# Optimization experiments

Measured on AMD Instinct MI355X. Metric: run time of the kernel, lower is better.

Reference implementation:

```python
import jax, jax.numpy as jnp
import numpy as np

N = 50000
E = 800000
IN_C, HID_C, OUT_C = 128, 256, 2


def sage_conv(x, src, dst, W_l, b_l, W_r, num_nodes):
    # PyG SAGEConv with mean aggregation:
    #   out = lin_l(mean_{j in N(i)} x_j) + lin_r(x_i)
    msg = x[src]                                            # [E, d] gather
    agg = jax.ops.segment_sum(msg, dst, num_segments=num_nodes)   # [N, d]
    cnt = jax.ops.segment_sum(jnp.ones((msg.shape[0],), x.dtype), dst,
                              num_segments=num_nodes)        # [N]
    agg = agg / jnp.maximum(cnt, 1.0)[:, None]               # mean (deg>=1)
    return agg @ W_l.T + b_l + x @ W_r.T


def setup_inputs() -> dict:
    key = jax.random.key(0)
    ks = jax.random.split(key, 8)
    x = jax.random.normal(ks[0], (N, IN_C), dtype=jnp.float32)
    edge_index = jax.random.randint(ks[1], (2, E), 0, N, dtype=jnp.int32)
    # glorot-ish scaled params
    s1 = 1.0 / np.sqrt(IN_C)
    s2 = 1.0 / np.sqrt(HID_C)
    W1l = jax.random.normal(ks[2], (HID_C, IN_C), dtype=jnp.float32) * s1
    W1r = jax.random.normal(ks[3], (HID_C, IN_C), dtype=jnp.float32) * s1
    b1 = jnp.zeros((HID_C,), dtype=jnp.float32)
    W2l = jax.random.normal(ks[4], (OUT_C, HID_C), dtype=jnp.float32) * s2
    W2r = jax.random.normal(ks[5], (OUT_C, HID_C), dtype=jnp.float32) * s2
    b2 = jnp.zeros((OUT_C,), dtype=jnp.float32)
    return {"x": x, "edge_index": edge_index,
            "W1l": W1l, "b1": b1, "W1r": W1r,
            "W2l": W2l, "b2": b2, "W2r": W2r}


def reference(x, edge_index, W1l, b1, W1r, W2l, b2, W2r):
    src, dst = edge_index[0], edge_index[1]
    h = sage_conv(x, src, dst, W1l, b1, W1r, N)
    h = jax.nn.relu(h)
    out = sage_conv(h, src, dst, W2l, b2, W2r, N)
    return out
```

## Files before the change

kernel.cpp:

```cpp
#include <hip/hip_runtime.h>
#include <hip/hip_bf16.h>


#define IN_C 128
#define HID_C 256
#define BKT_SHIFT 7
#define BKT_W 128
#define CAP 3072

typedef __attribute__((ext_vector_type(8))) short short8;
typedef __attribute__((ext_vector_type(4))) float f32x4;

static __device__ __forceinline__ unsigned short f2b(float f) {
    __hip_bfloat16 h = __float2bfloat16(f);
    return *(unsigned short*)&h;
}
static __device__ __forceinline__ float b2f(unsigned short u) {
    unsigned v = ((unsigned)u) << 16;
    return *(float*)&v;
}

__global__ __launch_bounds__(512) void scatter_conv(
    const float* __restrict__ x, unsigned int* __restrict__ Abf,
    const float* __restrict__ w1l, const float* __restrict__ w1r,
    unsigned short* __restrict__ Bg,
    const int* __restrict__ ei, int* __restrict__ bcnt,
    unsigned int* __restrict__ binned,
    int npairs , int xblk, int E_) {
    __shared__ int hist[512];
    __shared__ int lbase[512];
    const int tid = threadIdx.x;
    if (blockIdx.x < xblk) {
        int t = blockIdx.x * 512 + tid;
        if (t >= npairs) return;
        float2 v = *(const float2*)&x[(size_t)t * 2];
        unsigned int o = ((unsigned)f2b(v.y) << 16) | f2b(v.x);
        int node = t >> 6, g = t & 63;
        Abf[(size_t)node * 128 + 64 + g] = o;
    } else if (blockIdx.x < xblk + 128) {
        int idx = (blockIdx.x - xblk) * 512 + tid;
        int o = idx >> 8, k = idx & 255;
        float f = (k < IN_C) ? w1l[o * IN_C + k] : w1r[o * IN_C + (k - IN_C)];
        Bg[idx] = f2b(f);
    } else {
        const int e0 = (blockIdx.x - xblk - 128) * 2048;
        hist[tid] = 0;
        __syncthreads();
        int dreg[4];
#pragma unroll
        for (int j = 0; j < 4; ++j) {
            int e = e0 + j * 512 + tid;
            dreg[j] = (e < E_) ? ei[E_ + e] : -1;
            if (dreg[j] >= 0) atomicAdd(&hist[dreg[j] >> BKT_SHIFT], 1);
        }
        __syncthreads();
        {
            int c = hist[tid];
            lbase[tid] = c ? tid * CAP + atomicAdd(&bcnt[tid], c) : 0;
            hist[tid] = 0;
        }
        __syncthreads();
#pragma unroll
        for (int j = 0; j < 4; ++j) {
            int e = e0 + j * 512 + tid;
            if (dreg[j] >= 0) {
                int d = dreg[j];
                int b = d >> BKT_SHIFT;
                int pos = lbase[b] + atomicAdd(&hist[b], 1);
                if (pos < b * CAP + CAP)
                    binned[pos] = ((unsigned)ei[e] << BKT_SHIFT) |
                                  (unsigned)(d & (BKT_W - 1));
            }
        }
    }
}


__global__ __launch_bounds__(1024) void sort_gather(
    unsigned int* __restrict__ binned, const int* __restrict__ bcnt,
    const uint4* __restrict__ abf4c, uint4* __restrict__ Abf4,
    int* __restrict__ deg, int* __restrict__ boffs, int n) {
    __shared__ unsigned int ebuf[CAP];
    __shared__ unsigned short sbuf[CAP];
    __shared__ int hist[BKT_W];
    __shared__ int offs[BKT_W];
    __shared__ int cur[BKT_W];
    const int tid = threadIdx.x;
    const int lane = tid & 63;
    const int bkt = blockIdx.x;
    const int gbase = bkt * CAP;
    int cnt = bcnt[bkt];
    if (cnt > CAP) cnt = CAP;

    if (tid < BKT_W) hist[tid] = 0;
    {
        const int cnt4 = cnt >> 2;
        const uint4* b4 = (const uint4*)(binned + gbase);
        uint4* e4 = (uint4*)ebuf;
        for (int i = tid; i < cnt4; i += 1024) e4[i] = b4[i];
        for (int i = cnt4 * 4 + tid; i < cnt; i += 1024)
            ebuf[i] = binned[gbase + i];
    }
    __syncthreads();
    for (int i = tid; i < cnt; i += 1024)
        atomicAdd(&hist[ebuf[i] & (BKT_W - 1)], 1);
    __syncthreads();
    if (tid < 64) {
        int h0 = hist[lane * 2], h1 = hist[lane * 2 + 1];
        int s = h0 + h1;
        int incl = s;
#pragma unroll
        for (int off = 1; off < 64; off <<= 1) {
            int t = __shfl_up(incl, off);
            if (lane >= off) incl += t;
        }
        int excl = incl - s;
        offs[lane * 2] = excl;          cur[lane * 2] = excl;
        offs[lane * 2 + 1] = excl + h0; cur[lane * 2 + 1] = excl + h0;
    }
    __syncthreads();
    for (int i = tid; i < cnt; i += 1024) {
        unsigned int pk = ebuf[i];
        int pos = atomicAdd(&cur[pk & (BKT_W - 1)], 1);
        sbuf[pos] = (unsigned short)(pk >> BKT_SHIFT);
    }
    if (tid < BKT_W) {
        int node = bkt * BKT_W + tid;
        if (node < n) { deg[node] = hist[tid]; boffs[node] = offs[tid]; }
    }
    __syncthreads();

    {
        unsigned int* so = (unsigned int*)(binned + gbase);
        const int half = (cnt + 1) >> 1;
        for (int i = tid; i < half; i += 1024) {
            unsigned lo = sbuf[i * 2];
            unsigned hi = (i * 2 + 1 < cnt) ? sbuf[i * 2 + 1] : 0u;
            so[i] = lo | (hi << 16);
        }
    }

    const int wv = tid >> 6;
    const int ep = lane >> 4;
    const int pos = lane & 15;
    for (int ld = wv * 8; ld < wv * 8 + 8; ++ld) {
        int node = bkt * BKT_W + ld;
        if (node >= n) break;
        int beg = offs[ld], end = offs[ld] + hist[ld];
        float s[8] = {0.f, 0.f, 0.f, 0.f, 0.f, 0.f, 0.f, 0.f};
        for (int e = beg; e < end; e += 16) {
#pragma unroll
            for (int g = 0; g < 4; ++g) {
                int eg = e + g * 4 + ep;
                if (eg < end) {
                    int src = sbuf[eg];
                    uint4 u = abf4c[(size_t)src * 32 + 16 + pos];
                    s[0] += b2f(u.x & 0xffff); s[1] += b2f(u.x >> 16);
                    s[2] += b2f(u.y & 0xffff); s[3] += b2f(u.y >> 16);
                    s[4] += b2f(u.z & 0xffff); s[5] += b2f(u.z >> 16);
                    s[6] += b2f(u.w & 0xffff); s[7] += b2f(u.w >> 16);
                }
            }
        }
#pragma unroll
        for (int i = 0; i < 8; ++i) {
            s[i] += __shfl_xor(s[i], 16);
            s[i] += __shfl_xor(s[i], 32);
        }
        if (ep == 0) {
            float inv = 1.0f / (float)max(end - beg, 1);
            uint4 o;
            o.x = ((unsigned)f2b(s[1] * inv) << 16) | f2b(s[0] * inv);
            o.y = ((unsigned)f2b(s[3] * inv) << 16) | f2b(s[2] * inv);
            o.z = ((unsigned)f2b(s[5] * inv) << 16) | f2b(s[4] * inv);
            o.w = ((unsigned)f2b(s[7] * inv) << 16) | f2b(s[6] * inv);
            Abf4[(size_t)node * 32 + pos] = o;
        }
    }
}


#define LSTR 72

__global__ __launch_bounds__(256) void gemm1_fused(
    const unsigned short* __restrict__ Abf, const unsigned short* __restrict__ Bg,
    const float* __restrict__ b1, const float* __restrict__ w2l,
    const float* __restrict__ w2r, float* __restrict__ p2g,
    float* __restrict__ rsg, int nn) {
    __shared__ short As[128 * LSTR];
    __shared__ short Bs[128 * LSTR];

    const int tid = threadIdx.x;
    const int lane = tid & 63;
    const int wid = tid >> 6;
    const int wm = wid >> 1, wn = wid & 1;
    const int row0 = blockIdx.x * 128;
    const int col0 = blockIdx.y * 128;

    const int srow = tid >> 1;
    const int skc = (tid & 1) * 32;
    int arow = row0 + srow;
    if (arow >= nn) arow = nn - 1;
    const size_t agoff = (size_t)arow * 256 + skc;
    const size_t bgoff = (size_t)(col0 + srow) * 256 + skc;

    f32x4 acc[4][4];
#pragma unroll
    for (int i = 0; i < 4; ++i)
#pragma unroll
        for (int j = 0; j < 4; ++j) acc[i][j] = (f32x4){0.f, 0.f, 0.f, 0.f};

    const int quad = lane >> 4;
    const int l16 = lane & 15;

    for (int k0 = 0; k0 < 256; k0 += 64) {
        const uint4* ga = (const uint4*)(Abf + agoff + k0);
        const uint4* gb = (const uint4*)(Bg + bgoff + k0);
        uint4 va0 = ga[0], va1 = ga[1], va2 = ga[2], va3 = ga[3];
        uint4 vb0 = gb[0], vb1 = gb[1], vb2 = gb[2], vb3 = gb[3];

        __syncthreads();
        uint4* la = (uint4*)&As[srow * LSTR + skc];
        uint4* lb = (uint4*)&Bs[srow * LSTR + skc];
        la[0] = va0; la[1] = va1; la[2] = va2; la[3] = va3;
        lb[0] = vb0; lb[1] = vb1; lb[2] = vb2; lb[3] = vb3;
        __syncthreads();

#pragma unroll
        for (int kb = 0; kb < 2; ++kb) {
            short8 af[4], bf[4];
#pragma unroll
            for (int mt = 0; mt < 4; ++mt)
                af[mt] = *(const short8*)&As[(wm * 64 + mt * 16 + l16) * LSTR + kb * 32 + quad * 8];
#pragma unroll
            for (int nt = 0; nt < 4; ++nt)
                bf[nt] = *(const short8*)&Bs[(wn * 64 + nt * 16 + l16) * LSTR + kb * 32 + quad * 8];
#pragma unroll
            for (int mt = 0; mt < 4; ++mt)
#pragma unroll
                for (int nt = 0; nt < 4; ++nt)
                    acc[mt][nt] = __builtin_amdgcn_mfma_f32_16x16x32_bf16(
                        af[mt], bf[nt], acc[mt][nt], 0, 0, 0);
        }
    }

    const int cbase = col0 + wn * 64 + l16;
#pragma unroll
    for (int half = 0; half < 2; ++half) {
        const float* wA = half ? w2r : w2l;
        float* og = half ? rsg : p2g;
        f32x4 part[2][4];
#pragma unroll
        for (int c = 0; c < 2; ++c)
#pragma unroll
            for (int mt = 0; mt < 4; ++mt) part[c][mt] = (f32x4){0.f, 0.f, 0.f, 0.f};
#pragma unroll
        for (int nt = 0; nt < 4; ++nt) {
            const int col = cbase + nt * 16;
            const float bias = b1[col];
            const float w0 = wA[col];
            const float w1 = wA[HID_C + col];
#pragma unroll
            for (int mt = 0; mt < 4; ++mt)
#pragma unroll
                for (int r = 0; r < 4; ++r) {
                    float hv = fmaxf(acc[mt][nt][r] + bias, 0.0f);
                    part[0][mt][r] += hv * w0;
                    part[1][mt][r] += hv * w1;
                }
        }
#pragma unroll
        for (int c = 0; c < 2; ++c)
#pragma unroll
            for (int mt = 0; mt < 4; ++mt)
#pragma unroll
                for (int r = 0; r < 4; ++r)
#pragma unroll
                    for (int m = 1; m < 16; m <<= 1)
                        part[c][mt][r] += __shfl_xor(part[c][mt][r], m);
        if (l16 < 8) {
            const int ch2 = l16 & 1;
            const int mts = l16 >> 1;
#pragma unroll
            for (int r = 0; r < 4; ++r) {
                int row = row0 + wm * 64 + quad * 4 + mts * 16 + r;
                if (row < nn)
                    atomicAdd(&og[row * 2 + ch2], part[ch2][mts][r]);
            }
        }
    }
}


__global__ __launch_bounds__(512) void fin_bucket(
    const unsigned int* __restrict__ binned, const int* __restrict__ boffs,
    const int* __restrict__ deg,
    const float2* __restrict__ p2, const float2* __restrict__ rs,
    const float* __restrict__ b2, float* __restrict__ out, int n) {
    __shared__ float ps0[3][BKT_W];
    __shared__ float ps1[3][BKT_W];
    const int tid = threadIdx.x;
    const int ln = tid & (BKT_W - 1);
    const int hp = tid >> 7;
    const int bkt = blockIdx.x;
    const int node = bkt * BKT_W + ln;
    const unsigned short* sp =
        (const unsigned short*)(binned + (size_t)bkt * CAP);
    float s0 = 0.f, s1 = 0.f;
    int dg = 0;
    if (node < n) {
        int beg = boffs[node];
        dg = deg[node];
        int end = beg + dg;
        for (int i = beg + hp; i < end; i += 4) {
            float2 v = p2[sp[i]];
            s0 += v.x; s1 += v.y;
        }
    }
    if (hp) { ps0[hp - 1][ln] = s0; ps1[hp - 1][ln] = s1; }
    __syncthreads();
    if (!hp && node < n) {
        s0 += ps0[0][ln] + ps0[1][ln] + ps0[2][ln];
        s1 += ps1[0][ln] + ps1[1][ln] + ps1[2][ln];
        float inv = 1.0f / (float)max(dg, 1);
        float2 self = rs[node];
        out[node * 2 + 0] = s0 * inv + self.x + b2[0];
        out[node * 2 + 1] = s1 * inv + self.y + b2[1];
    }
}


extern "C" void kernel_launch(void* const* d_in, const int* in_sizes, int n_in,
                              void* d_out, int out_size, void* d_ws, size_t ws_size,
                              hipStream_t stream) {
    const float* x   = (const float*)d_in[0];
    const int*   ei  = (const int*)d_in[1];
    const float* W1l = (const float*)d_in[2];
    const float* b1  = (const float*)d_in[3];
    const float* W1r = (const float*)d_in[4];
    const float* W2l = (const float*)d_in[5];
    const float* b2  = (const float*)d_in[6];
    const float* W2r = (const float*)d_in[7];
    float* out = (float*)d_out;

    const int N_ = in_sizes[0] / IN_C;
    const int E_ = in_sizes[1] / 2;
    const int nbkt = (N_ + BKT_W - 1) / BKT_W;

    char* wsb = (char*)d_ws;
    size_t off = 0;
    auto alloc = [&](size_t bytes) {
        void* ptr = wsb + off;
        off += ((bytes + 15) & ~(size_t)15);
        return ptr;
    };
    unsigned short* Abf = (unsigned short*)alloc((size_t)N_ * 256 * 2);
    unsigned short* Bg  = (unsigned short*)alloc(256 * 256 * 2);
    unsigned int* binned = (unsigned int*)alloc((size_t)(nbkt + 1) * CAP * 4);
    int*   bcnt = (int*)alloc(512 * 4);
    float* p2f  = (float*)alloc((size_t)N_ * 2 * 4);
    float* rsf  = (float*)alloc((size_t)N_ * 2 * 4);
    int*   deg  = (int*)alloc((size_t)N_ * 4);
    int*   boffs = (int*)alloc((size_t)N_ * 4);

    const int xblk = (N_ * 64 + 511) / 512;
    const int eblk = (E_ + 2047) / 2048;

    hipMemsetAsync(bcnt, 0, 512 * sizeof(int) + (size_t)N_ * 2 * 4 * 2, stream);

    scatter_conv<<<xblk + 128 + eblk, 512, 0, stream>>>(
        x, (unsigned int*)Abf, W1l, W1r, Bg, ei, bcnt, binned,
        N_ * 64, xblk, E_);

    sort_gather<<<nbkt, 1024, 0, stream>>>(binned, bcnt, (const uint4*)Abf,
                                           (uint4*)Abf, deg, boffs, N_);

    gemm1_fused<<<dim3((N_ + 127) / 128, 2), 256, 0, stream>>>(
        Abf, Bg, b1, W2l, W2r, p2f, rsf, N_);

    fin_bucket<<<nbkt, 512, 0, stream>>>(binned, boffs, deg,
                                         (const float2*)p2f, (const float2*)rsf,
                                         b2, out, N_);
}
```

Before: 182.0 us.

## Vectorize bf16 conversion, prefetch next GEMM K-tile, remap block order

The x and weight bf16 conversion paths now use float4 loads with wider stores, so fewer blocks are launched for that phase. The layer-1 GEMM prefetches the next K-tile's global data into registers while MFMA runs on the current tile. A 1D grid remaps blocks so both column tiles of a row group are scheduled close together, which should improve L2 reuse of A. This costs extra registers for the prefetch and makes the index math more complex.

```diff
diff --git a/kernel.cpp b/kernel.cpp
--- a/kernel.cpp
+++ b/kernel.cpp
@@ -26,24 +26,30 @@
     unsigned short* __restrict__ Bg,
     const int* __restrict__ ei, int* __restrict__ bcnt,
     unsigned int* __restrict__ binned,
-    int npairs , int xblk, int E_) {
+    int nquads , int xblk, int E_) {
     __shared__ int hist[512];
     __shared__ int lbase[512];
     const int tid = threadIdx.x;
     if (blockIdx.x < xblk) {
         int t = blockIdx.x * 512 + tid;
-        if (t >= npairs) return;
-        float2 v = *(const float2*)&x[(size_t)t * 2];
-        unsigned int o = ((unsigned)f2b(v.y) << 16) | f2b(v.x);
-        int node = t >> 6, g = t & 63;
-        Abf[(size_t)node * 128 + 64 + g] = o;
-    } else if (blockIdx.x < xblk + 128) {
-        int idx = (blockIdx.x - xblk) * 512 + tid;
-        int o = idx >> 8, k = idx & 255;
-        float f = (k < IN_C) ? w1l[o * IN_C + k] : w1r[o * IN_C + (k - IN_C)];
-        Bg[idx] = f2b(f);
+        if (t >= nquads) return;
+        float4 v = *(const float4*)&x[(size_t)t * 4];
+        uint2 o;
+        o.x = ((unsigned)f2b(v.y) << 16) | f2b(v.x);
+        o.y = ((unsigned)f2b(v.w) << 16) | f2b(v.z);
+        int node = t >> 5, g = t & 31;
+        *(uint2*)&Abf[(size_t)node * 128 + 64 + g * 2] = o;
+    } else if (blockIdx.x < xblk + 32) {
+        int idx4 = (blockIdx.x - xblk) * 512 + tid;
+        int o = idx4 >> 6, k4 = (idx4 & 63) * 4;
+        const float* srcp = (k4 < IN_C) ? &w1l[o * IN_C + k4]
+                                        : &w1r[o * IN_C + (k4 - IN_C)];
+        float4 f = *(const float4*)srcp;
+        ushort4 s;
+        s.x = f2b(f.x); s.y = f2b(f.y); s.z = f2b(f.z); s.w = f2b(f.w);
+        *(ushort4*)&Bg[(size_t)idx4 * 4] = s;
     } else {
-        const int e0 = (blockIdx.x - xblk - 128) * 2048;
+        const int e0 = (blockIdx.x - xblk - 32) * 2048;
         hist[tid] = 0;
         __syncthreads();
         int dreg[4];
@@ -186,16 +192,28 @@
     const unsigned short* __restrict__ Abf, const unsigned short* __restrict__ Bg,
     const float* __restrict__ b1, const float* __restrict__ w2l,
     const float* __restrict__ w2r, float* __restrict__ p2g,
-    float* __restrict__ rsg, int nn) {
+    float* __restrict__ rsg, int nn, int full16) {
     __shared__ short As[128 * LSTR];
     __shared__ short Bs[128 * LSTR];
+
+    int idx = blockIdx.x;
+    int rowt, colt;
+    if (idx < full16) {
+        int g = idx >> 4, r = idx & 15;
+        rowt = g * 8 + (r & 7);
+        colt = r >> 3;
+    } else {
+        int r2 = idx - full16;
+        rowt = (full16 >> 1) + (r2 >> 1);
+        colt = r2 & 1;
+    }
+    const int row0 = rowt * 128;
+    const int col0 = colt * 128;
 
     const int tid = threadIdx.x;
     const int lane = tid & 63;
     const int wid = tid >> 6;
     const int wm = wid >> 1, wn = wid & 1;
-    const int row0 = blockIdx.x * 128;
-    const int col0 = blockIdx.y * 128;
 
     const int srow = tid >> 1;
     const int skc = (tid & 1) * 32;
@@ -213,18 +231,28 @@
     const int quad = lane >> 4;
     const int l16 = lane & 15;
 
+    uint4 va0, va1, va2, va3, vb0, vb1, vb2, vb3;
+    {
+        const uint4* ga = (const uint4*)(Abf + agoff);
+        const uint4* gb = (const uint4*)(Bg + bgoff);
+        va0 = ga[0]; va1 = ga[1]; va2 = ga[2]; va3 = ga[3];
+        vb0 = gb[0]; vb1 = gb[1]; vb2 = gb[2]; vb3 = gb[3];
+    }
+
     for (int k0 = 0; k0 < 256; k0 += 64) {
-        const uint4* ga = (const uint4*)(Abf + agoff + k0);
-        const uint4* gb = (const uint4*)(Bg + bgoff + k0);
-        uint4 va0 = ga[0], va1 = ga[1], va2 = ga[2], va3 = ga[3];
-        uint4 vb0 = gb[0], vb1 = gb[1], vb2 = gb[2], vb3 = gb[3];
-
         __syncthreads();
         uint4* la = (uint4*)&As[srow * LSTR + skc];
         uint4* lb = (uint4*)&Bs[srow * LSTR + skc];
         la[0] = va0; la[1] = va1; la[2] = va2; la[3] = va3;
         lb[0] = vb0; lb[1] = vb1; lb[2] = vb2; lb[3] = vb3;
         __syncthreads();
+
+        if (k0 + 64 < 256) {
+            const uint4* ga = (const uint4*)(Abf + agoff + k0 + 64);
+            const uint4* gb = (const uint4*)(Bg + bgoff + k0 + 64);
+            va0 = ga[0]; va1 = ga[1]; va2 = ga[2]; va3 = ga[3];
+            vb0 = gb[0]; vb1 = gb[1]; vb2 = gb[2]; vb3 = gb[3];
+        }
 
 #pragma unroll
         for (int kb = 0; kb < 2; ++kb) {
@@ -363,20 +391,22 @@
     int*   deg  = (int*)alloc((size_t)N_ * 4);
     int*   boffs = (int*)alloc((size_t)N_ * 4);
 
-    const int xblk = (N_ * 64 + 511) / 512;
+    const int xblk = (N_ * 32 + 511) / 512;
     const int eblk = (E_ + 2047) / 2048;
 
     hipMemsetAsync(bcnt, 0, 512 * sizeof(int) + (size_t)N_ * 2 * 4 * 2, stream);
 
-    scatter_conv<<<xblk + 128 + eblk, 512, 0, stream>>>(
+    scatter_conv<<<xblk + 32 + eblk, 512, 0, stream>>>(
         x, (unsigned int*)Abf, W1l, W1r, Bg, ei, bcnt, binned,
-        N_ * 64, xblk, E_);
+        N_ * 32, xblk, E_);
 
     sort_gather<<<nbkt, 1024, 0, stream>>>(binned, bcnt, (const uint4*)Abf,
                                            (uint4*)Abf, deg, boffs, N_);
 
-    gemm1_fused<<<dim3((N_ + 127) / 128, 2), 256, 0, stream>>>(
-        Abf, Bg, b1, W2l, W2r, p2f, rsf, N_);
+    const int nbx = (N_ + 127) / 128;
+    const int full16 = (nbx / 8) * 16;
+    gemm1_fused<<<nbx * 2, 256, 0, stream>>>(
+        Abf, Bg, b1, W2l, W2r, p2f, rsf, N_, full16);
 
     fin_bucket<<<nbkt, 512, 0, stream>>>(binned, boffs, deg,
                                          (const float2*)p2f, (const float2*)rsf,
```

Result: slower. 191.2 us (+5.0%).
